# Kernel optimization log

Measured on AMD Instinct MI355X. Metric: run time of the kernel, lower is better.

The kernel has to match this reference:

```python
import jax, jax.numpy as jnp
import numpy as np

N = 4096      # nodes
E = 65536     # edges (avg degree 16)
NNIN = 64; NEIN = 64; NOPEN = 128; NHID = 128; NCLOSE = 128; NLAYER = 4
H = 0.1; NUM_OUT = 1024; LIN_HID = 256; EPS = 1e-5


def ln_all(x):
    # F.layer_norm(x, x.shape): normalize over ALL elements, no affine
    m = jnp.mean(x)
    v = jnp.mean((x - m) ** 2)
    return (x - m) * jax.lax.rsqrt(v + EPS)


def double_layer(x, K1, K2):
    # edgeConv with 2-D kernel == 1x1 conv == channel mixing
    x = jnp.einsum('oc,bcn->bon', K1, x)
    x = jnp.tanh(ln_all(x))
    return jnp.einsum('oc,bcn->bon', K2, x)


def node_grad(x, I, J, w):      # [1,C,N] -> [1,C,E]
    return w * (x[:, :, I] - x[:, :, J])


def node_ave(x, I, J, w):
    return 0.5 * w * (x[:, :, I] + x[:, :, J])


def edge_div(g, I, J, w, n):    # [1,C,E] -> [1,C,N], signed scatter-add
    wg = w * g
    z = jnp.zeros(g.shape[:2] + (n,), g.dtype)
    return z.at[:, :, I].add(wg).at[:, :, J].add(-wg)


def edge_ave(g, I, J, w, n):    # method='ave'
    wg = w * g
    z = jnp.zeros(g.shape[:2] + (n,), g.dtype)
    return 0.5 * (z.at[:, :, I].add(wg) + z.at[:, :, J].add(wg))


def setup_inputs():
    key = jax.random.key(0)
    ks = jax.random.split(key, 20)
    stdv = 1e-3
    nfeat = 3 * NOPEN  # varlet=False
    return {
        'xn': jax.random.normal(ks[0], (1, NNIN, N), jnp.float32),
        'xe': jax.random.normal(ks[1], (1, NEIN, E), jnp.float32),
        'iInd': jax.random.randint(ks[2], (E,), 0, N),
        'jInd': jax.random.randint(ks[3], (E,), 0, N),
        'K1Nopen': jax.random.normal(ks[4], (NOPEN, NNIN)) * stdv,
        'K2Nopen': jax.random.normal(ks[5], (NOPEN, NOPEN)) * stdv,
        'K1Eopen': jax.random.normal(ks[6], (NOPEN, NEIN)) * stdv,
        'K2Eopen': jax.random.normal(ks[7], (NOPEN, NOPEN)) * stdv,
        'KNclose': jax.random.normal(ks[8], (NCLOSE, NOPEN)) * stdv,
        'KE1': jax.random.uniform(ks[9], (NLAYER, NHID, nfeat)) * stdv,
        'KE2': jax.random.uniform(ks[10], (NLAYER, NOPEN, NHID)) * stdv,
        'KN1': jax.random.uniform(ks[11], (NLAYER, NHID, nfeat)) * stdv,
        'KN2': jax.random.uniform(ks[12], (NLAYER, NOPEN, NHID)) * stdv,
        'W1': jax.random.normal(ks[13], (LIN_HID, NCLOSE)) * 0.02,
        'b1': jnp.zeros((LIN_HID,), jnp.float32),
        'W2': jax.random.normal(ks[14], (NUM_OUT, LIN_HID)) * 0.02,
        'b2': jnp.zeros((NUM_OUT,), jnp.float32),
    }


def reference(xn, xe, iInd, jInd, K1Nopen, K2Nopen, K1Eopen, K2Eopen, KNclose,
              KE1, KE2, KN1, KN2, W1, b1, W2, b2):
    xn = double_layer(xn, K1Nopen, K2Nopen)
    xe = double_layer(xe, K1Eopen, K2Eopen)
    for i in range(NLAYER):
        # periodic pairwise-distance graph reweighting (cdist-style)
        f = xn[0]                                    # [C, N]
        s = jnp.sum(f * f, axis=0)                   # [N]
        D = jax.nn.relu(s[None, :] + s[:, None] - 2.0 * (f.T @ f))  # [N, N]
        D = jnp.exp(-2.0 * D / jnp.std(D, ddof=1))   # torch .std() is unbiased
        w = D[iInd, jInd]                            # [E]
        gradX = node_grad(xn, iInd, jInd, w)
        intX = node_ave(xn, iInd, jInd, w)
        dxe = jnp.concatenate([intX, xe, gradX], axis=1)     # [1, 3*nopen, E]
        dxe = ln_all(double_layer(dxe, KE1[i], KE2[i]))
        xe = xe + H * dxe                                    # wave=True
        divE = edge_div(xe, iInd, jInd, w, N)
        aveE = edge_ave(xe, iInd, jInd, w, N)
        dxn = jnp.concatenate([aveE, divE, xn], axis=1)      # [1, 3*nopen, N]
        dxn = double_layer(dxn, KN1[i], KN2[i])
        xn = xn + H * dxn
    xn = jnp.einsum('oc,bcn->bon', KNclose, xn)  # 1x1 conv close
    x = xn[0].T                                  # [N, nNclose]
    x = jax.nn.elu(x @ W1.T + b1)
    x = x @ W2.T + b2
    return jax.nn.log_softmax(x, axis=1)
```

## Files before the change

### kernel.cpp

```cpp
#include <hip/hip_runtime.h>

#define NNODES 4096
#define NEDGES 65536
#define CH 128

typedef __bf16 bf16x8_t __attribute__((ext_vector_type(8)));
typedef __bf16 bf16x4_t __attribute__((ext_vector_type(4)));
typedef __bf16 bf16x2_t __attribute__((ext_vector_type(2)));
typedef float f32x4_t __attribute__((ext_vector_type(4)));

__device__ __forceinline__ float fast_tanh(float x)
{
  float t = __builtin_amdgcn_exp2f(x * 2.885390081777927f);
  return 1.f - 2.f * __builtin_amdgcn_rcpf(t + 1.f);
}

__device__ __forceinline__ void write_stats(float s, float q, float2* __restrict__ partials,
                                            int pid, int tid, int nwaves)
{
#pragma unroll
  for (int d = 1; d < 64; d <<= 1) { s += __shfl_xor(s, d); q += __shfl_xor(q, d); }
  __shared__ float rs[8][2];
  const int wv = tid >> 6, lane = tid & 63;
  if (lane == 0) { rs[wv][0] = s; rs[wv][1] = q; }
  __syncthreads();
  if (tid == 0) {
    float S = 0.f, Q = 0.f;
    for (int i = 0; i < nwaves; ++i) { S += rs[i][0]; Q += rs[i][1]; }
    partials[pid] = {S, Q};
  }
}

__device__ __forceinline__ float2 params_inline(const float2* __restrict__ pp,
                                                int nblk, double M, int type)
{
  const int tid = threadIdx.x;
  double s = 0.0, q = 0.0;
  for (int i = tid; i < nblk; i += 256) { float2 v = pp[i]; s += (double)v.x; q += (double)v.y; }
#pragma unroll
  for (int d = 1; d < 64; d <<= 1) { s += __shfl_xor(s, d); q += __shfl_xor(q, d); }
  __shared__ double rs4[4], rq4[4];
  __shared__ float pr[2];
  const int wv = tid >> 6, lane = tid & 63;
  if (lane == 0) { rs4[wv] = s; rq4[wv] = q; }
  __syncthreads();
  if (tid == 0) {
    double S = rs4[0] + rs4[1] + rs4[2] + rs4[3];
    double Q = rq4[0] + rq4[1] + rq4[2] + rq4[3];
    if (type == 0) {
      double mean = S / M;
      double var = Q / M - mean * mean;
      if (var < 0.0) var = 0.0;
      pr[0] = (float)mean;
      pr[1] = (float)(1.0 / sqrt(var + 1e-5));
    } else {
      double var = (Q - S * S / M) / (M - 1.0);
      if (var < 1e-30) var = 1e-30;
      pr[0] = (float)(-2.0 / sqrt(var));
      pr[1] = 0.f;
    }
  }
  __syncthreads();
  return {pr[0], pr[1]};
}

template<int EM, int K, int OBS, bool WPH>
__global__ __launch_bounds__(256) void emfma_k(
    const __bf16* __restrict__ A, const __bf16* __restrict__ X,
    __bf16* __restrict__ Cb,
    float2* __restrict__ partials,
    const __bf16* __restrict__ UVb, const __bf16* __restrict__ xnNb,
    const float* __restrict__ sbufh,
    const int* __restrict__ iI, const int* __restrict__ jJ,
    float* __restrict__ wbuf, const float2* __restrict__ pD,
    const float2* __restrict__ pp, int pnblk, double pM)
{
  __shared__ float wl[64];
  __shared__ int il[64], jl[64];
  const int tid = threadIdx.x;
  const int wv = tid >> 6, lane = tid & 63;
  const int l15 = lane & 15, ks = lane >> 4;
  const int row = wv * 16 + l15;
  const int e = blockIdx.x * 64 + row;
  constexpr int KK = K / 32;
  bf16x8_t bq[KK];
  {
    const __bf16* xr = X + (size_t)e * K + ks * 8;
#pragma unroll
    for (int kk = 0; kk < KK; ++kk) bq[kk] = *(const bf16x8_t*)(xr + kk * 32);
  }
  if constexpr (WPH) {
    double s = 0.0, q = 0.0;
    for (int i = tid; i < 2080; i += 256) { float2 v = pD[i]; s += (double)v.x; q += (double)v.y; }
    const int eg = blockIdx.x * 64 + (tid >> 2);
    const int a = iI[eg], b = jJ[eg];
    if ((tid & 3) == 0) { il[tid >> 2] = a; jl[tid >> 2] = b; }
    const bf16x8_t* pa = (const bf16x8_t*)(xnNb + (size_t)a * CH + (tid & 3) * 32);
    const bf16x8_t* pb = (const bf16x8_t*)(xnNb + (size_t)b * CH + (tid & 3) * 32);
    float g = 0.f;
#pragma unroll
    for (int q4 = 0; q4 < 4; ++q4) {
      bf16x8_t u = pa[q4], v = pb[q4];
#pragma unroll
      for (int j = 0; j < 8; ++j) g = fmaf((float)u[j], (float)v[j], g);
    }
    g += __shfl_xor(g, 1); g += __shfl_xor(g, 2);
    float dd = sbufh[a] + sbufh[NNODES + a] + sbufh[b] + sbufh[NNODES + b] - 2.f * g;
    dd = dd > 0.f ? dd : 0.f;
#pragma unroll
    for (int d = 1; d < 64; d <<= 1) { s += __shfl_xor(s, d); q += __shfl_xor(q, d); }
    __shared__ double rs4[4], rq4[4];
    __shared__ float prf;
    if (lane == 0) { rs4[wv] = s; rq4[wv] = q; }
    __syncthreads();
    if (tid == 0) {
      double S = rs4[0] + rs4[1] + rs4[2] + rs4[3];
      double Q = rq4[0] + rq4[1] + rq4[2] + rq4[3];
      const double M = (double)NNODES * (double)NNODES;
      double var = (Q - S * S / M) / (M - 1.0);
      if (var < 1e-30) var = 1e-30;
      prf = (float)(-2.0 / sqrt(var));
    }
    __syncthreads();
    float wgt = __builtin_amdgcn_exp2f(prf * dd * 1.4426950408889634f);
    if ((tid & 3) == 0) {
      wl[tid >> 2] = wgt;
      if (blockIdx.y == 0) wbuf[eg] = wgt;
    }
    __syncthreads();
  }
  if constexpr (EM == 1 || EM == 3) {
    float2 pr = params_inline(pp, pnblk, pM, 0);
    const float p0 = pr.x, p1 = pr.y;
#pragma unroll
    for (int kk = 0; kk < KK; ++kk) {
#pragma unroll
      for (int j = 0; j < 8; ++j)
        bq[kk][j] = (__bf16)fast_tanh(((float)bq[kk][j] - p0) * p1);
    }
  }
  float we = 0.f; int ie = 0, je = 0;
  if constexpr (EM == 2) { we = wl[row]; ie = il[row]; je = jl[row]; }
  float dsum = 0.f, dsq = 0.f;
  const int ob0 = blockIdx.y * OBS;
#pragma unroll
  for (int obb = 0; obb < OBS; ++obb) {
    const int ob = ob0 + obb;
    f32x4_t acc = {0.f, 0.f, 0.f, 0.f};
    const __bf16* ar = A + (size_t)(ob * 16 + l15) * K + ks * 8;
#pragma unroll
    for (int kk = 0; kk < KK; ++kk) {
      bf16x8_t a = *(const bf16x8_t*)(ar + kk * 32);
      acc = __builtin_amdgcn_mfma_f32_16x16x32_bf16(a, bq[kk], acc, 0, 0, 0);
    }
    const int ro = ob * 16 + ks * 4;
    float v0 = acc[0], v1 = acc[1], v2 = acc[2], v3 = acc[3];
    if constexpr (EM == 2) {
      bf16x4_t u4 = *(const bf16x4_t*)&UVb[(size_t)ie * 256 + ro];
      bf16x4_t w4 = *(const bf16x4_t*)&UVb[(size_t)je * 256 + 128 + ro];
      v0 += we * ((float)u4[0] + (float)w4[0]);
      v1 += we * ((float)u4[1] + (float)w4[1]);
      v2 += we * ((float)u4[2] + (float)w4[2]);
      v3 += we * ((float)u4[3] + (float)w4[3]);
    }
    if constexpr (EM != 3) {
      dsum += v0 + v1 + v2 + v3;
      dsq  += v0 * v0 + v1 * v1 + v2 * v2 + v3 * v3;
    }
    bf16x4_t bv;
    bv[0] = (__bf16)v0; bv[1] = (__bf16)v1; bv[2] = (__bf16)v2; bv[3] = (__bf16)v3;
    *(bf16x4_t*)(Cb + (size_t)e * 128 + ro) = bv;
  }
  if constexpr (EM != 3)
    write_stats(dsum, dsq, partials, blockIdx.y * gridDim.x + blockIdx.x, tid, 4);
}

template<int K, bool XSPLIT, bool XT, bool STATS, int OM, bool EMITB, int OBS>
__global__ __launch_bounds__(256) void nmfma_k(
    const __bf16* __restrict__ A, const __bf16* __restrict__ X,
    const __bf16* __restrict__ X2,
    __bf16* __restrict__ Cb, float* __restrict__ Cf, float* __restrict__ resid,
    const float* __restrict__ bias, int nout_stride,
    float2* __restrict__ partials,
    const float2* __restrict__ pp, int pnblk, double pM,
    __bf16* __restrict__ xbout, float* __restrict__ shout)
{
  const int tid = threadIdx.x;
  const int wv = tid >> 6, lane = tid & 63;
  const int l15 = lane & 15, ks = lane >> 4;
  const int n = blockIdx.x * 64 + wv * 16 + l15;
  constexpr int KK = K / 32;
  bf16x8_t bq[KK];
  if constexpr (XSPLIT) {
    const __bf16* xr  = X  + (size_t)n * 256 + ks * 8;
    const __bf16* xr2 = X2 + (size_t)n * 128 + ks * 8;
#pragma unroll
    for (int kk = 0; kk < 8; ++kk) bq[kk] = *(const bf16x8_t*)(xr + kk * 32);
#pragma unroll
    for (int kk = 8; kk < KK; ++kk) bq[kk] = *(const bf16x8_t*)(xr2 + (kk - 8) * 32);
  } else {
    const __bf16* xr = X + (size_t)n * K + ks * 8;
#pragma unroll
    for (int kk = 0; kk < KK; ++kk) bq[kk] = *(const bf16x8_t*)(xr + kk * 32);
  }
  if constexpr (XT) {
    float2 pr = params_inline(pp, pnblk, pM, 0);
    const float p0 = pr.x, p1 = pr.y;
#pragma unroll
    for (int kk = 0; kk < KK; ++kk) {
#pragma unroll
      for (int j = 0; j < 8; ++j)
        bq[kk][j] = (__bf16)fast_tanh(((float)bq[kk][j] - p0) * p1);
    }
  }
  float dsum = 0.f, dsq = 0.f, ss = 0.f;
  const int ob0 = blockIdx.y * OBS;
#pragma unroll
  for (int obb = 0; obb < OBS; ++obb) {
    const int ob = ob0 + obb;
    f32x4_t acc = {0.f, 0.f, 0.f, 0.f};
    const __bf16* ar = A + (size_t)(ob * 16 + l15) * K + ks * 8;
#pragma unroll
    for (int kk = 0; kk < KK; ++kk) {
      bf16x8_t a = *(const bf16x8_t*)(ar + kk * 32);
      acc = __builtin_amdgcn_mfma_f32_16x16x32_bf16(a, bq[kk], acc, 0, 0, 0);
    }
    const int ro = ob * 16 + ks * 4;
    float v[4] = {acc[0], acc[1], acc[2], acc[3]};
    if constexpr (OM == 1 || OM == 2) {
#pragma unroll
      for (int r = 0; r < 4; ++r) v[r] += bias[ro + r];
    }
    if constexpr (OM == 1) {
#pragma unroll
      for (int r = 0; r < 4; ++r) v[r] = v[r] > 0.f ? v[r] : expm1f(v[r]);
    }
    if constexpr (STATS) {
#pragma unroll
      for (int r = 0; r < 4; ++r) { dsum += v[r]; dsq += v[r] * v[r]; }
    }
    if constexpr (OM == 4) {
      float4* rp = (float4*)&resid[(size_t)n * 128 + ro];
      float4 rr = *rp;
      rr.x += 0.1f * v[0]; rr.y += 0.1f * v[1]; rr.z += 0.1f * v[2]; rr.w += 0.1f * v[3];
      *rp = rr;
      if constexpr (EMITB) {
        bf16x4_t eb;
        eb[0] = (__bf16)rr.x; eb[1] = (__bf16)rr.y; eb[2] = (__bf16)rr.z; eb[3] = (__bf16)rr.w;
        *(bf16x4_t*)(xbout + (size_t)n * 128 + ro) = eb;
#pragma unroll
        for (int r = 0; r < 4; ++r) { float f = (float)eb[r]; ss += f * f; }
      }
    } else if constexpr (OM == 2 || OM == 3) {
      float4 fv = {v[0], v[1], v[2], v[3]};
      *(float4*)(Cf + (size_t)n * nout_stride + ro) = fv;
      if constexpr (EMITB) {
        bf16x4_t eb;
        eb[0] = (__bf16)v[0]; eb[1] = (__bf16)v[1]; eb[2] = (__bf16)v[2]; eb[3] = (__bf16)v[3];
        *(bf16x4_t*)(xbout + (size_t)n * 128 + ro) = eb;
#pragma unroll
        for (int r = 0; r < 4; ++r) { float f = (float)eb[r]; ss += f * f; }
      }
    } else {
      bf16x4_t bv;
      bv[0] = (__bf16)v[0]; bv[1] = (__bf16)v[1]; bv[2] = (__bf16)v[2]; bv[3] = (__bf16)v[3];
      *(bf16x4_t*)(Cb + (size_t)n * nout_stride + ro) = bv;
    }
  }
  if constexpr (EMITB) {
    ss += __shfl_xor(ss, 16);
    ss += __shfl_xor(ss, 32);
    if (lane < 16) shout[blockIdx.y * NNODES + n] = ss;
  }
  if constexpr (STATS)
    write_stats(dsum, dsq, partials, blockIdx.y * gridDim.x + blockIdx.x, tid, 4);
}

__global__ __launch_bounds__(256) void dstat_k(
    const __bf16* __restrict__ fT, const float* __restrict__ sh,
    float2* __restrict__ partials)
{
  int rem = blockIdx.x, i0t = 0;
  while (rem >= 64 - i0t) { rem -= 64 - i0t; ++i0t; }
  const int i0 = i0t * 64, j0 = (i0t + rem) * 64;
  const float wgt = (j0 > i0) ? 2.f : 1.f;
  const int tid = threadIdx.x;
  const int wv = tid >> 6, lane = tid & 63, l15 = lane & 15, ks = lane >> 4;
  const int irow = i0 + wv * 16 + l15;
  bf16x8_t aq[4];
  const __bf16* ar = fT + (size_t)irow * 128 + ks * 8;
#pragma unroll
  for (int kk = 0; kk < 4; ++kk) aq[kk] = *(const bf16x8_t*)(ar + kk * 32);
  float si[4];
#pragma unroll
  for (int r = 0; r < 4; ++r) {
    int ii = i0 + wv * 16 + ks * 4 + r;
    si[r] = sh[ii] + sh[NNODES + ii];
  }
  float dsum = 0.f, dsq = 0.f;
#pragma unroll
  for (int jb = 0; jb < 4; ++jb) {
    const int jcol = j0 + jb * 16 + l15;
    const __bf16* br = fT + (size_t)jcol * 128 + ks * 8;
    f32x4_t acc = {0.f, 0.f, 0.f, 0.f};
#pragma unroll
    for (int kk = 0; kk < 4; ++kk) {
      bf16x8_t b = *(const bf16x8_t*)(br + kk * 32);
      acc = __builtin_amdgcn_mfma_f32_16x16x32_bf16(aq[kk], b, acc, 0, 0, 0);
    }
    const float sj = sh[jcol] + sh[NNODES + jcol];
#pragma unroll
    for (int r = 0; r < 4; ++r) {
      float d = si[r] + sj - 2.f * acc[r];
      d = d > 0.f ? d : 0.f;
      dsum += d; dsq += d * d;
    }
  }
  write_stats(dsum * wgt, dsq * wgt, partials, blockIdx.x, tid, 4);
}

__global__ __launch_bounds__(256) void etrans_k(const float* __restrict__ src,
                                                __bf16* __restrict__ dst, int ncols)
{
  __shared__ float t[64][65];
  const int e0 = blockIdx.x * 64;
  const int tx = threadIdx.x & 63, tw = threadIdx.x >> 6;
  for (int c = tw; c < 64; c += 4)
    t[tx][c] = src[(size_t)c * ncols + e0 + tx];
  __syncthreads();
  const int el = threadIdx.x >> 2, c0 = (threadIdx.x & 3) * 16;
  for (int q = 0; q < 4; ++q) {
    int c = c0 + q * 4;
    bf16x4_t b;
    b[0] = (__bf16)t[el][c];     b[1] = (__bf16)t[el][c + 1];
    b[2] = (__bf16)t[el][c + 2]; b[3] = (__bf16)t[el][c + 3];
    *(bf16x4_t*)&dst[(size_t)(e0 + el) * 64 + c] = b;
  }
}

__global__ void wcvt_k(const float* __restrict__ K1E, const float* __restrict__ K2E,
                       const float* __restrict__ KE1, const float* __restrict__ KE2,
                       const float* __restrict__ KNc, const float* __restrict__ W1,
                       const float* __restrict__ W2, const float* __restrict__ KN1,
                       const float* __restrict__ KN2, const float* __restrict__ K1N,
                       const float* __restrict__ K2N,
                       __bf16* __restrict__ K1Eb, __bf16* __restrict__ K2Eb,
                       __bf16* __restrict__ KE1b, __bf16* __restrict__ KE2b,
                       __bf16* __restrict__ KNcb, __bf16* __restrict__ W1b,
                       __bf16* __restrict__ W2b, __bf16* __restrict__ KN1b,
                       __bf16* __restrict__ KN2b, __bf16* __restrict__ a1a2b,
                       __bf16* __restrict__ K1Nb, __bf16* __restrict__ K2Nb)
{
  int id = blockIdx.x * 256 + threadIdx.x;
  if (id < 8192) { K1Eb[id] = (__bf16)K1E[id]; return; }
  id -= 8192;
  if (id < 16384) { K2Eb[id] = (__bf16)K2E[id]; return; }
  id -= 16384;
  if (id < 65536) {
    int l = id >> 14, rem = id & 16383, r = rem >> 7, c = rem & 127;
    KE1b[id] = (__bf16)KE1[(size_t)l * 49152 + r * 384 + 128 + c];
    return;
  }
  id -= 65536;
  if (id < 65536) { KE2b[id] = (__bf16)KE2[id]; return; }
  id -= 65536;
  if (id < 16384) { KNcb[id] = (__bf16)KNc[id]; return; }
  id -= 16384;
  if (id < 32768) { W1b[id] = (__bf16)W1[id]; return; }
  id -= 32768;
  if (id < 262144) { W2b[id] = (__bf16)W2[id]; return; }
  id -= 262144;
  if (id < 196608) { KN1b[id] = (__bf16)KN1[id]; return; }
  id -= 196608;
  if (id < 65536) { KN2b[id] = (__bf16)KN2[id]; return; }
  id -= 65536;
  if (id < 131072) {
    int l = id >> 15, rem = id & 32767, r = rem >> 7, c = rem & 127;
    int o = r & 127;
    float k1 = KE1[(size_t)l * 49152 + o * 384 + c];
    float k3 = KE1[(size_t)l * 49152 + o * 384 + 256 + c];
    a1a2b[id] = (__bf16)((r < 128) ? (0.5f * k1 + k3) : (0.5f * k1 - k3));
    return;
  }
  id -= 131072;
  if (id < 8192) { K1Nb[id] = (__bf16)K1N[id]; return; }
  id -= 8192;
  if (id < 16384) { K2Nb[id] = (__bf16)K2N[id]; return; }
}

__global__ __launch_bounds__(256) void lnres_k(
    const __bf16* __restrict__ eBT, __bf16* __restrict__ xeT,
    const float2* __restrict__ pp, int pnblk)
{
  const size_t base = (size_t)blockIdx.x * (256 * 16);
  const size_t i0 = base + (size_t)threadIdx.x * 8;
  const size_t i1 = i0 + 2048;
  bf16x8_t b0 = *(const bf16x8_t*)(eBT + i0);
  bf16x8_t x0 = *(const bf16x8_t*)(xeT + i0);
  bf16x8_t b1 = *(const bf16x8_t*)(eBT + i1);
  bf16x8_t x1 = *(const bf16x8_t*)(xeT + i1);
  float2 pr = params_inline(pp, pnblk, (double)CH * NEDGES, 0);
  const float m = pr.x, r = pr.y;
  bf16x8_t o0, o1;
#pragma unroll
  for (int j = 0; j < 8; ++j) {
    o0[j] = (__bf16)((float)x0[j] + 0.1f * (((float)b0[j] - m) * r));
    o1[j] = (__bf16)((float)x1[j] + 0.1f * (((float)b1[j] - m) * r));
  }
  *(bf16x8_t*)(xeT + i0) = o0;
  *(bf16x8_t*)(xeT + i1) = o1;
}

__global__ void hist_k(const int* __restrict__ iI, const int* __restrict__ jJ,
                       int* __restrict__ cnt)
{
  int e = blockIdx.x * 256 + threadIdx.x;
  atomicAdd(&cnt[iI[e]], 1);
  atomicAdd(&cnt[jJ[e]], 1);
}

__global__ __launch_bounds__(1024) void scan_k(const int* __restrict__ cnt,
                                               int* __restrict__ offs,
                                               int* __restrict__ cursor)
{
  __shared__ int tmp[1024];
  const int tid = threadIdx.x;
  int4 v = *(const int4*)&cnt[tid * 4];
  int s = v.x + v.y + v.z + v.w;
  tmp[tid] = s; __syncthreads();
  for (int d = 1; d < 1024; d <<= 1) {
    int t = (tid >= d) ? tmp[tid - d] : 0;
    __syncthreads();
    tmp[tid] += t;
    __syncthreads();
  }
  int base = tmp[tid] - s;
  int4 o = {base, base + v.x, base + v.x + v.y, base + v.x + v.y + v.z};
  *(int4*)&offs[tid * 4] = o;
  *(int4*)&cursor[tid * 4] = o;
  if (tid == 1023) offs[4096] = tmp[1023];
}

__global__ void fill_k(const int* __restrict__ iI, const int* __restrict__ jJ,
                       int* __restrict__ cursor, int* __restrict__ list)
{
  int e = blockIdx.x * 256 + threadIdx.x;
  int p1 = atomicAdd(&cursor[iI[e]], 1);
  list[p1] = e;
  int p2 = atomicAdd(&cursor[jJ[e]], 1);
  list[p2] = e | 0x80000000;
}

__global__ __launch_bounds__(512) void gather_k(
    const __bf16* __restrict__ xeT, const float* __restrict__ w,
    const int* __restrict__ offs, const int* __restrict__ list,
    __bf16* __restrict__ catb)
{
  __shared__ float comb[4][4][64];
  const int wv = threadIdx.x >> 6, lane = threadIdx.x & 63;
  const int nn = wv >> 1, half = wv & 1;
  const int n = blockIdx.x * 4 + nn;
  const int k0 = offs[n], k1 = offs[n + 1];
  float s1a = 0.f, s1b = 0.f, s2a = 0.f, s2b = 0.f;
#pragma unroll 2
  for (int k = k0 + half; k < k1; k += 2) {
    int enc = list[k];
    int e = enc & 0x7fffffff;
    float we = w[e];
    bf16x2_t xv = *(const bf16x2_t*)&xeT[(size_t)e * 128 + lane * 2];
    float va = (float)xv[0] * we;
    float vb = (float)xv[1] * we;
    if (enc >= 0) { s1a += va; s1b += vb; }
    else          { s2a += va; s2b += vb; }
  }
  if (half == 1) {
    comb[nn][0][lane] = s1a; comb[nn][1][lane] = s1b;
    comb[nn][2][lane] = s2a; comb[nn][3][lane] = s2b;
  }
  __syncthreads();
  if (half == 0) {
    s1a += comb[nn][0][lane]; s1b += comb[nn][1][lane];
    s2a += comb[nn][2][lane]; s2b += comb[nn][3][lane];
    __bf16* row = catb + (size_t)n * 256;
    bf16x2_t av, dv;
    av[0] = (__bf16)(0.5f * (s1a + s2a)); av[1] = (__bf16)(0.5f * (s1b + s2b));
    dv[0] = (__bf16)(s1a - s2a);          dv[1] = (__bf16)(s1b - s2b);
    *(bf16x2_t*)&row[lane * 2] = av;
    *(bf16x2_t*)&row[128 + lane * 2] = dv;
  }
}

__global__ __launch_bounds__(256) void logsoftmax_k(float* __restrict__ out)
{
  __shared__ float red[256];
  const int n = blockIdx.x, tid = threadIdx.x;
  float* row = out + (size_t)n * 1024;
  float v[4];
  float mx = -1e30f;
#pragma unroll
  for (int l = 0; l < 4; ++l) { v[l] = row[tid + 256 * l]; mx = fmaxf(mx, v[l]); }
  red[tid] = mx; __syncthreads();
  for (int s = 128; s > 0; s >>= 1) { if (tid < s) red[tid] = fmaxf(red[tid], red[tid + s]); __syncthreads(); }
  float m = red[0]; __syncthreads();
  float se = 0.f;
#pragma unroll
  for (int l = 0; l < 4; ++l) se += expf(v[l] - m);
  red[tid] = se; __syncthreads();
  for (int s = 128; s > 0; s >>= 1) { if (tid < s) red[tid] += red[tid + s]; __syncthreads(); }
  float L = m + logf(red[0]);
#pragma unroll
  for (int l = 0; l < 4; ++l) row[tid + 256 * l] = v[l] - L;
}

extern "C" void kernel_launch(void* const* d_in, const int* in_sizes, int n_in,
                              void* d_out, int out_size, void* d_ws, size_t ws_size,
                              hipStream_t stream)
{
  (void)in_sizes; (void)n_in; (void)out_size; (void)ws_size;
  const float* xn_in = (const float*)d_in[0];
  const float* xe_in = (const float*)d_in[1];
  const int*   iI    = (const int*)d_in[2];
  const int*   jJ    = (const int*)d_in[3];
  const float* K1N   = (const float*)d_in[4];
  const float* K2N   = (const float*)d_in[5];
  const float* K1E   = (const float*)d_in[6];
  const float* K2E   = (const float*)d_in[7];
  const float* KNc   = (const float*)d_in[8];
  const float* KE1   = (const float*)d_in[9];
  const float* KE2   = (const float*)d_in[10];
  const float* KN1   = (const float*)d_in[11];
  const float* KN2   = (const float*)d_in[12];
  const float* W1    = (const float*)d_in[13];
  const float* b1    = (const float*)d_in[14];
  const float* W2    = (const float*)d_in[15];
  const float* b2    = (const float*)d_in[16];
  float* out = (float*)d_out;

  float* ws = (float*)d_ws;
  size_t off = 0;
  auto alloc = [&](size_t n) { size_t o = off; off += (n + 63) & ~(size_t)63; return o; };
  float* xnN   = ws + alloc((size_t)NNODES * CH);
  __bf16* xeT  = (__bf16*)(ws + alloc((size_t)NEDGES * CH / 2));
  __bf16* eAT  = (__bf16*)(ws + alloc((size_t)NEDGES * CH / 2));
  __bf16* eBT  = (__bf16*)(ws + alloc((size_t)NEDGES * CH / 2));
  float* sbufh = ws + alloc(2 * NNODES);
  float* wbuf  = ws + alloc(NEDGES);
  __bf16* UVb  = (__bf16*)(ws + alloc((size_t)NNODES * 256 / 2));
  __bf16* xnNb = (__bf16*)(ws + alloc((size_t)NNODES * CH / 2));
  __bf16* catb = (__bf16*)(ws + alloc((size_t)NNODES * 256 / 2));
  __bf16* nAb  = (__bf16*)(ws + alloc((size_t)NNODES * CH / 2));
  __bf16* zb   = (__bf16*)(ws + alloc((size_t)NNODES * CH / 2));
  __bf16* l1bb = (__bf16*)(ws + alloc((size_t)NNODES * 256 / 2));
  __bf16* K1Eb = (__bf16*)(ws + alloc(8192 / 2));
  __bf16* K2Eb = (__bf16*)(ws + alloc(16384 / 2));
  __bf16* KE1b = (__bf16*)(ws + alloc(65536 / 2));
  __bf16* KE2b = (__bf16*)(ws + alloc(65536 / 2));
  __bf16* KNcb = (__bf16*)(ws + alloc(16384 / 2));
  __bf16* W1b  = (__bf16*)(ws + alloc(32768 / 2));
  __bf16* W2b  = (__bf16*)(ws + alloc(262144 / 2));
  __bf16* KN1b = (__bf16*)(ws + alloc(196608 / 2));
  __bf16* KN2b = (__bf16*)(ws + alloc(65536 / 2));
  __bf16* a1a2b= (__bf16*)(ws + alloc(131072 / 2));
  __bf16* K1Nb = (__bf16*)(ws + alloc(8192 / 2));
  __bf16* K2Nb = (__bf16*)(ws + alloc(16384 / 2));
  int* csr_cnt    = (int*)(ws + alloc(4096));
  int* csr_offs   = (int*)(ws + alloc(4160));
  int* csr_cursor = (int*)(ws + alloc(4096));
  int* csr_list   = (int*)(ws + alloc(2 * NEDGES));
  float2* pA = (float2*)(ws + alloc((size_t)4096 * 2));
  float2* pB = (float2*)(ws + alloc((size_t)4096 * 2));
  float2* pC = (float2*)(ws + alloc((size_t)4096 * 2));
  __bf16* xeT64  = eBT;
  __bf16* xnT64b = UVb;

  const __bf16* BNUL = nullptr;
  const float* NUL = nullptr;
  const int* NULI = nullptr;
  const float2* PNUL = nullptr;
  __bf16* BNULm = nullptr;
  float* NULm = nullptr;
  float* FNULm = nullptr;

  wcvt_k<<<3456, 256, 0, stream>>>(K1E, K2E, KE1, KE2, KNc, W1, W2, KN1, KN2, K1N, K2N,
                                   K1Eb, K2Eb, KE1b, KE2b, KNcb, W1b, W2b, KN1b, KN2b,
                                   a1a2b, K1Nb, K2Nb);
  hipMemsetAsync(csr_cnt, 0, 4096 * sizeof(int), stream);
  hist_k<<<NEDGES / 256, 256, 0, stream>>>(iI, jJ, csr_cnt);
  scan_k<<<1, 1024, 0, stream>>>(csr_cnt, csr_offs, csr_cursor);
  fill_k<<<NEDGES / 256, 256, 0, stream>>>(iI, jJ, csr_cursor, csr_list);

  etrans_k<<<NNODES / 64, 256, 0, stream>>>(xn_in, xnT64b, NNODES);
  nmfma_k<64, false, false, true, 0, false, 1><<<dim3(64, 8), 256, 0, stream>>>(
      K1Nb, xnT64b, BNUL, nAb, nullptr, nullptr, NUL, 128, pA, PNUL, 0, 0.0, BNULm, NULm);
  nmfma_k<128, false, true, false, 3, true, 4><<<dim3(64, 2), 256, 0, stream>>>(
      K2Nb, nAb, BNUL, nullptr, xnN, nullptr, NUL, 128, nullptr,
      pA, 512, (double)CH * NNODES, xnNb, sbufh);

  etrans_k<<<NEDGES / 64, 256, 0, stream>>>(xe_in, xeT64, NEDGES);
  emfma_k<0, 64, 4, false><<<dim3(NEDGES / 64, 2), 256, 0, stream>>>(
      K1Eb, xeT64, eAT, pA, BNUL, BNUL, NUL, NULI, NULI, FNULm, PNUL, PNUL, 0, 0.0);
  emfma_k<3, 128, 4, false><<<dim3(NEDGES / 64, 2), 256, 0, stream>>>(
      K2Eb, eAT, xeT, nullptr, BNUL, BNUL, NUL, NULI, NULI, FNULm, PNUL,
      pA, 2048, (double)CH * NEDGES);

  for (int i = 0; i < 4; ++i) {
    const __bf16* KE1bi = KE1b + (size_t)i * 128 * 128;
    const __bf16* KE2bi = KE2b + (size_t)i * 128 * 128;
    const __bf16* KN1bi = KN1b + (size_t)i * 128 * 384;
    const __bf16* KN2bi = KN2b + (size_t)i * 128 * 128;
    const __bf16* a1a2i = a1a2b + (size_t)i * 256 * 128;

    dstat_k<<<2080, 256, 0, stream>>>(xnNb, sbufh, pA);

    nmfma_k<128, false, false, false, 0, false, 1><<<dim3(64, 16), 256, 0, stream>>>(
        a1a2i, xnNb, BNUL, UVb, nullptr, nullptr, NUL, 256, nullptr, PNUL, 0, 0.0, BNULm, NULm);

    emfma_k<2, 128, 4, true><<<dim3(NEDGES / 64, 2), 256, 0, stream>>>(
        KE1bi, xeT, eAT, pB, UVb, xnNb, sbufh, iI, jJ, wbuf, pA, PNUL, 0, 0.0);
    emfma_k<1, 128, 4, false><<<dim3(NEDGES / 64, 2), 256, 0, stream>>>(
        KE2bi, eAT, eBT, pC, BNUL, BNUL, NUL, NULI, NULI, FNULm, PNUL,
        pB, 2048, (double)CH * NEDGES);
    lnres_k<<<2048, 256, 0, stream>>>(eBT, xeT, pC, 2048);

    gather_k<<<NNODES / 4, 512, 0, stream>>>(xeT, wbuf, csr_offs, csr_list, catb);
    nmfma_k<384, true, false, true, 0, false, 1><<<dim3(64, 8), 256, 0, stream>>>(
        KN1bi, catb, xnNb, nAb, nullptr, nullptr, NUL, 128, pB, PNUL, 0, 0.0, BNULm, NULm);
    nmfma_k<128, false, true, false, 4, true, 4><<<dim3(64, 2), 256, 0, stream>>>(
        KN2bi, nAb, BNUL, nullptr, nullptr, xnN, NUL, 128, nullptr,
        pB, 512, (double)CH * NNODES, xnNb, sbufh);
  }

  nmfma_k<128, false, false, false, 0, false, 1><<<dim3(64, 8), 256, 0, stream>>>(
      KNcb, xnNb, BNUL, zb, nullptr, nullptr, NUL, 128, nullptr, PNUL, 0, 0.0, BNULm, NULm);
  nmfma_k<128, false, false, false, 1, false, 1><<<dim3(64, 16), 256, 0, stream>>>(
      W1b, zb, BNUL, l1bb, nullptr, nullptr, b1, 256, nullptr, PNUL, 0, 0.0, BNULm, NULm);
  nmfma_k<256, false, false, false, 2, false, 1><<<dim3(64, 64), 256, 0, stream>>>(
      W2b, l1bb, BNUL, nullptr, out, nullptr, b2, 1024, nullptr, PNUL, 0, 0.0, BNULm, NULm);
  logsoftmax_k<<<NNODES, 256, 0, stream>>>(out);
}
```

Measured before the change: 676.4 us.

## Process four edge groups per block in edge MFMA kernels

The edge MFMA kernel now handles 256 edges per block (EPB=4) instead of 64, so each block reuses its weight tile across four edge groups and the grid shrinks fourfold. This also cuts the number of stats partials from 2048 to 512, which lowers the reduction cost in the downstream consumers. In the weight phase, each thread now computes a full 128-channel dot product per edge instead of four threads sharing one edge with shuffles. The cost is higher register pressure from holding four sets of B fragments (KK=4 gives 16 vectors), and fewer blocks (512) to fill the GPU.

```diff
diff --git a/kernel.cpp b/kernel.cpp
--- a/kernel.cpp
+++ b/kernel.cpp
@@ -64,7 +64,7 @@
   return {pr[0], pr[1]};
 }
 
-template<int EM, int K, int OBS, bool WPH>
+template<int EM, int K, int OBS, bool WPH, int EPB>
 __global__ __launch_bounds__(256) void emfma_k(
     const __bf16* __restrict__ A, const __bf16* __restrict__ X,
     __bf16* __restrict__ Cb,
@@ -75,37 +75,47 @@
     float* __restrict__ wbuf, const float2* __restrict__ pD,
     const float2* __restrict__ pp, int pnblk, double pM)
 {
-  __shared__ float wl[64];
-  __shared__ int il[64], jl[64];
+  __shared__ float wl[64 * EPB];
+  __shared__ int il[64 * EPB], jl[64 * EPB];
   const int tid = threadIdx.x;
   const int wv = tid >> 6, lane = tid & 63;
   const int l15 = lane & 15, ks = lane >> 4;
   const int row = wv * 16 + l15;
-  const int e = blockIdx.x * 64 + row;
+  const int base_e = blockIdx.x * 64 * EPB;
   constexpr int KK = K / 32;
-  bf16x8_t bq[KK];
-  {
-    const __bf16* xr = X + (size_t)e * K + ks * 8;
-#pragma unroll
-    for (int kk = 0; kk < KK; ++kk) bq[kk] = *(const bf16x8_t*)(xr + kk * 32);
+  bf16x8_t bq[EPB][KK];
+#pragma unroll
+  for (int g = 0; g < EPB; ++g) {
+    const __bf16* xr = X + (size_t)(base_e + g * 64 + row) * K + ks * 8;
+#pragma unroll
+    for (int kk = 0; kk < KK; ++kk) bq[g][kk] = *(const bf16x8_t*)(xr + kk * 32);
   }
   if constexpr (WPH) {
+    static_assert(EPB == 4, "WPH assumes 256 edges/block");
     double s = 0.0, q = 0.0;
     for (int i = tid; i < 2080; i += 256) { float2 v = pD[i]; s += (double)v.x; q += (double)v.y; }
-    const int eg = blockIdx.x * 64 + (tid >> 2);
+    const int eg = base_e + tid;
     const int a = iI[eg], b = jJ[eg];
-    if ((tid & 3) == 0) { il[tid >> 2] = a; jl[tid >> 2] = b; }
-    const bf16x8_t* pa = (const bf16x8_t*)(xnNb + (size_t)a * CH + (tid & 3) * 32);
-    const bf16x8_t* pb = (const bf16x8_t*)(xnNb + (size_t)b * CH + (tid & 3) * 32);
-    float g = 0.f;
-#pragma unroll
-    for (int q4 = 0; q4 < 4; ++q4) {
-      bf16x8_t u = pa[q4], v = pb[q4];
-#pragma unroll
-      for (int j = 0; j < 8; ++j) g = fmaf((float)u[j], (float)v[j], g);
-    }
-    g += __shfl_xor(g, 1); g += __shfl_xor(g, 2);
-    float dd = sbufh[a] + sbufh[NNODES + a] + sbufh[b] + sbufh[NNODES + b] - 2.f * g;
+    il[tid] = a; jl[tid] = b;
+    const bf16x8_t* pa = (const bf16x8_t*)(xnNb + (size_t)a * CH);
+    const bf16x8_t* pb = (const bf16x8_t*)(xnNb + (size_t)b * CH);
+    float g0 = 0.f, g1 = 0.f, g2 = 0.f, g3 = 0.f;
+#pragma unroll
+    for (int q16 = 0; q16 < 16; q16 += 4) {
+      bf16x8_t u0 = pa[q16],     v0 = pb[q16];
+      bf16x8_t u1 = pa[q16 + 1], v1 = pb[q16 + 1];
+      bf16x8_t u2 = pa[q16 + 2], v2 = pb[q16 + 2];
+      bf16x8_t u3 = pa[q16 + 3], v3 = pb[q16 + 3];
+#pragma unroll
+      for (int j = 0; j < 8; ++j) {
+        g0 = fmaf((float)u0[j], (float)v0[j], g0);
+        g1 = fmaf((float)u1[j], (float)v1[j], g1);
+        g2 = fmaf((float)u2[j], (float)v2[j], g2);
+        g3 = fmaf((float)u3[j], (float)v3[j], g3);
+      }
+    }
+    float gg = (g0 + g1) + (g2 + g3);
+    float dd = sbufh[a] + sbufh[NNODES + a] + sbufh[b] + sbufh[NNODES + b] - 2.f * gg;
     dd = dd > 0.f ? dd : 0.f;
 #pragma unroll
     for (int d = 1; d < 64; d <<= 1) { s += __shfl_xor(s, d); q += __shfl_xor(q, d); }
@@ -123,53 +133,57 @@
     }
     __syncthreads();
     float wgt = __builtin_amdgcn_exp2f(prf * dd * 1.4426950408889634f);
-    if ((tid & 3) == 0) {
-      wl[tid >> 2] = wgt;
-      if (blockIdx.y == 0) wbuf[eg] = wgt;
-    }
+    wl[tid] = wgt;
+    if (blockIdx.y == 0) wbuf[eg] = wgt;
     __syncthreads();
   }
   if constexpr (EM == 1 || EM == 3) {
     float2 pr = params_inline(pp, pnblk, pM, 0);
     const float p0 = pr.x, p1 = pr.y;
 #pragma unroll
-    for (int kk = 0; kk < KK; ++kk) {
-#pragma unroll
-      for (int j = 0; j < 8; ++j)
-        bq[kk][j] = (__bf16)fast_tanh(((float)bq[kk][j] - p0) * p1);
-    }
-  }
-  float we = 0.f; int ie = 0, je = 0;
-  if constexpr (EM == 2) { we = wl[row]; ie = il[row]; je = jl[row]; }
+    for (int g = 0; g < EPB; ++g)
+#pragma unroll
+      for (int kk = 0; kk < KK; ++kk) {
+#pragma unroll
+        for (int j = 0; j < 8; ++j)
+          bq[g][kk][j] = (__bf16)fast_tanh(((float)bq[g][kk][j] - p0) * p1);
+      }
+  }
   float dsum = 0.f, dsq = 0.f;
   const int ob0 = blockIdx.y * OBS;
 #pragma unroll
-  for (int obb = 0; obb < OBS; ++obb) {
-    const int ob = ob0 + obb;
-    f32x4_t acc = {0.f, 0.f, 0.f, 0.f};
-    const __bf16* ar = A + (size_t)(ob * 16 + l15) * K + ks * 8;
-#pragma unroll
-    for (int kk = 0; kk < KK; ++kk) {
-      bf16x8_t a = *(const bf16x8_t*)(ar + kk * 32);
-      acc = __builtin_amdgcn_mfma_f32_16x16x32_bf16(a, bq[kk], acc, 0, 0, 0);
-    }
-    const int ro = ob * 16 + ks * 4;
-    float v0 = acc[0], v1 = acc[1], v2 = acc[2], v3 = acc[3];
-    if constexpr (EM == 2) {
-      bf16x4_t u4 = *(const bf16x4_t*)&UVb[(size_t)ie * 256 + ro];
-      bf16x4_t w4 = *(const bf16x4_t*)&UVb[(size_t)je * 256 + 128 + ro];
-      v0 += we * ((float)u4[0] + (float)w4[0]);
-      v1 += we * ((float)u4[1] + (float)w4[1]);
-      v2 += we * ((float)u4[2] + (float)w4[2]);
-      v3 += we * ((float)u4[3] + (float)w4[3]);
-    }
-    if constexpr (EM != 3) {
-      dsum += v0 + v1 + v2 + v3;
-      dsq  += v0 * v0 + v1 * v1 + v2 * v2 + v3 * v3;
-    }
-    bf16x4_t bv;
-    bv[0] = (__bf16)v0; bv[1] = (__bf16)v1; bv[2] = (__bf16)v2; bv[3] = (__bf16)v3;
-    *(bf16x4_t*)(Cb + (size_t)e * 128 + ro) = bv;
+  for (int g = 0; g < EPB; ++g) {
+    const int e = base_e + g * 64 + row;
+    float we = 0.f; int ie = 0, je = 0;
+    if constexpr (EM == 2) { we = wl[g * 64 + row]; ie = il[g * 64 + row]; je = jl[g * 64 + row]; }
+#pragma unroll
+    for (int obb = 0; obb < OBS; ++obb) {
+      const int ob = ob0 + obb;
+      f32x4_t acc = {0.f, 0.f, 0.f, 0.f};
+      const __bf16* ar = A + (size_t)(ob * 16 + l15) * K + ks * 8;
+#pragma unroll
+      for (int kk = 0; kk < KK; ++kk) {
+        bf16x8_t a = *(const bf16x8_t*)(ar + kk * 32);
+        acc = __builtin_amdgcn_mfma_f32_16x16x32_bf16(a, bq[g][kk], acc, 0, 0, 0);
+      }
+      const int ro = ob * 16 + ks * 4;
+      float v0 = acc[0], v1 = acc[1], v2 = acc[2], v3 = acc[3];
+      if constexpr (EM == 2) {
+        bf16x4_t u4 = *(const bf16x4_t*)&UVb[(size_t)ie * 256 + ro];
+        bf16x4_t w4 = *(const bf16x4_t*)&UVb[(size_t)je * 256 + 128 + ro];
+        v0 += we * ((float)u4[0] + (float)w4[0]);
+        v1 += we * ((float)u4[1] + (float)w4[1]);
+        v2 += we * ((float)u4[2] + (float)w4[2]);
+        v3 += we * ((float)u4[3] + (float)w4[3]);
+      }
+      if constexpr (EM != 3) {
+        dsum += v0 + v1 + v2 + v3;
+        dsq  += v0 * v0 + v1 * v1 + v2 * v2 + v3 * v3;
+      }
+      bf16x4_t bv;
+      bv[0] = (__bf16)v0; bv[1] = (__bf16)v1; bv[2] = (__bf16)v2; bv[3] = (__bf16)v3;
+      *(bf16x4_t*)(Cb + (size_t)e * 128 + ro) = bv;
+    }
   }
   if constexpr (EM != 3)
     write_stats(dsum, dsq, partials, blockIdx.y * gridDim.x + blockIdx.x, tid, 4);
@@ -597,11 +611,11 @@
       pA, 512, (double)CH * NNODES, xnNb, sbufh);
 
   etrans_k<<<NEDGES / 64, 256, 0, stream>>>(xe_in, xeT64, NEDGES);
-  emfma_k<0, 64, 4, false><<<dim3(NEDGES / 64, 2), 256, 0, stream>>>(
+  emfma_k<0, 64, 4, false, 4><<<dim3(NEDGES / 256, 2), 256, 0, stream>>>(
       K1Eb, xeT64, eAT, pA, BNUL, BNUL, NUL, NULI, NULI, FNULm, PNUL, PNUL, 0, 0.0);
-  emfma_k<3, 128, 4, false><<<dim3(NEDGES / 64, 2), 256, 0, stream>>>(
+  emfma_k<3, 128, 4, false, 4><<<dim3(NEDGES / 256, 2), 256, 0, stream>>>(
       K2Eb, eAT, xeT, nullptr, BNUL, BNUL, NUL, NULI, NULI, FNULm, PNUL,
-      pA, 2048, (double)CH * NEDGES);
+      pA, 512, (double)CH * NEDGES);
 
   for (int i = 0; i < 4; ++i) {
     const __bf16* KE1bi = KE1b + (size_t)i * 128 * 128;
@@ -615,12 +629,12 @@
     nmfma_k<128, false, false, false, 0, false, 1><<<dim3(64, 16), 256, 0, stream>>>(
         a1a2i, xnNb, BNUL, UVb, nullptr, nullptr, NUL, 256, nullptr, PNUL, 0, 0.0, BNULm, NULm);
 
-    emfma_k<2, 128, 4, true><<<dim3(NEDGES / 64, 2), 256, 0, stream>>>(
+    emfma_k<2, 128, 4, true, 4><<<dim3(NEDGES / 256, 2), 256, 0, stream>>>(
         KE1bi, xeT, eAT, pB, UVb, xnNb, sbufh, iI, jJ, wbuf, pA, PNUL, 0, 0.0);
-    emfma_k<1, 128, 4, false><<<dim3(NEDGES / 64, 2), 256, 0, stream>>>(
+    emfma_k<1, 128, 4, false, 4><<<dim3(NEDGES / 256, 2), 256, 0, stream>>>(
         KE2bi, eAT, eBT, pC, BNUL, BNUL, NUL, NULI, NULI, FNULm, PNUL,
-        pB, 2048, (double)CH * NEDGES);
-    lnres_k<<<2048, 256, 0, stream>>>(eBT, xeT, pC, 2048);
+        pB, 512, (double)CH * NEDGES);
+    lnres_k<<<2048, 256, 0, stream>>>(eBT, xeT, pC, 512);
 
     gather_k<<<NNODES / 4, 512, 0, stream>>>(xeT, wbuf, csr_offs, csr_list, catb);
     nmfma_k<384, true, false, true, 0, false, 1><<<dim3(64, 8), 256, 0, stream>>>(
```

After: 666.4 us. Within noise of the previous version (-1.5%).
